# Kernel optimization log

Hardware: AMD Instinct MI355X
Metric: run time of the kernel (lower is better)

Reference implementation:

```python
import jax, jax.numpy as jnp
import numpy as np

BETA = 0.3        # SmoothL1Loss beta
LAMBDA_PHY = 0.15 # physics loss weight


def smooth_l1(d, beta):
    ad = jnp.abs(d)
    return jnp.where(ad < beta, 0.5 * d * d / beta, ad - 0.5 * beta)


def setup_inputs() -> dict:
    key = jax.random.key(0)
    k1, k2, k3, k4 = jax.random.split(key, 4)
    B, Z = 16384, 2048
    preds = jax.random.normal(k1, (B, Z, 1), dtype=jnp.float32)
    targets = jax.random.normal(k2, (B, Z), dtype=jnp.float32)
    current_temps = jax.random.normal(k3, (B, Z), dtype=jnp.float32)
    adjacency = jax.random.randint(k4, (Z, Z), 0, 2).astype(jnp.int32)
    return {"preds": preds, "targets": targets,
            "current_temps": current_temps, "adjacency": adjacency}


def reference(preds, targets, current_temps, adjacency):
    p = preds[:, :, 0]                               # [B, Z]
    num_zones = p.shape[1]
    pred_loss = smooth_l1(p - targets, BETA).mean()
    pred_change = p - current_temps                  # [B, Z]

    # Vectorized neighbor mean: replaces the per-zone Python loop with one
    # dense masked-adjacency contraction.
    mask = (adjacency > 0).astype(p.dtype)           # [Z, Z]
    deg = mask.sum(axis=1)                           # [Z]
    has_nb = deg > 0
    safe_deg = jnp.where(has_nb, deg, 1.0)
    avg_neighbor = jnp.einsum('zn,bn->bz', mask, current_temps) / safe_deg  # [B, Z]

    temp_diff = current_temps - avg_neighbor         # [B, Z]
    violation = jax.nn.softplus(temp_diff * pred_change)
    per_zone = violation.mean(axis=0)                # mean over batch, [Z]
    physics_loss = jnp.where(has_nb, per_zone, 0.0).sum() / num_zones

    total_loss = pred_loss + LAMBDA_PHY * physics_loss
    return (total_loss, physics_loss)
```

## Files before the change

### kernel.cpp

```cpp
#include <hip/hip_runtime.h>
#include <hip/hip_bf16.h>
#include <cmath>

#define BETA 0.3f
#define LAMBDA_PHY 0.15f

#define BM 128
#define BN 128
#define BK 64
#define NT 512

typedef __bf16 bf16x8 __attribute__((ext_vector_type(8)));
typedef float f32x4 __attribute__((ext_vector_type(4)));

#define AS1 __attribute__((address_space(1)))
#define AS3 __attribute__((address_space(3)))

#define FENCE() asm volatile("" ::: "memory")
#define BARRIER() do { FENCE(); __builtin_amdgcn_s_barrier(); FENCE(); } while (0)
#define WAITV4() asm volatile("s_waitcnt vmcnt(4)" ::: "memory")
#define WAITV0() asm volatile("s_waitcnt vmcnt(0)" ::: "memory")

__device__ __forceinline__ unsigned short f2bf_rn(float f) {
    unsigned int u = __builtin_bit_cast(unsigned int, f);
    return (unsigned short)((u + 0x7FFFu + ((u >> 16) & 1u)) >> 16);
}

__device__ __forceinline__ float bf2f(unsigned short u) {
    return __builtin_bit_cast(float, (unsigned int)u << 16);
}

__device__ __forceinline__ float softplus_f(float x) {
    return fmaxf(x, 0.0f) + __logf(1.0f + __expf(-fabsf(x)));
}

__device__ __forceinline__ float smooth_l1_f(float d) {
    float ad = fabsf(d);
    return (ad < BETA) ? (0.5f / BETA) * d * d : (ad - 0.5f * BETA);
}

__global__ void k_prep(const int* __restrict__ adj, unsigned short* __restrict__ maskbf,
                       float* __restrict__ invdeg, float* __restrict__ hasnb, int Z) {
    int z = blockIdx.x;
    int t = threadIdx.x;
    const int* row = adj + (size_t)z * Z;
    unsigned short* mrow = maskbf + (size_t)z * Z;
    int cnt = 0;
    for (int n = t; n < Z; n += blockDim.x) {
        int a = (row[n] > 0);
        mrow[n] = a ? (unsigned short)0x3F80 : (unsigned short)0;
        cnt += a;
    }
    for (int o = 32; o; o >>= 1) cnt += __shfl_down(cnt, o);
    __shared__ int rs[4];
    int lane = t & 63, wave = t >> 6;
    if (lane == 0) rs[wave] = cnt;
    __syncthreads();
    if (t == 0) {
        int deg = rs[0] + rs[1] + rs[2] + rs[3];
        invdeg[z] = (deg > 0) ? 1.0f / (float)deg : 1.0f;
        hasnb[z]  = (deg > 0) ? 1.0f : 0.0f;
    }
}

__global__ void k_conv(const float* __restrict__ src, uint4* __restrict__ dst, long n8) {
    long i = (long)blockIdx.x * blockDim.x + threadIdx.x;
    long stride = (long)gridDim.x * blockDim.x;
    for (; i < n8; i += stride) {
        const float4* s = (const float4*)(src + i * 8);
        float4 a = s[0], b = s[1];
        uint4 o;
        o.x = (unsigned)f2bf_rn(a.x) | ((unsigned)f2bf_rn(a.y) << 16);
        o.y = (unsigned)f2bf_rn(a.z) | ((unsigned)f2bf_rn(a.w) << 16);
        o.z = (unsigned)f2bf_rn(b.x) | ((unsigned)f2bf_rn(b.y) << 16);
        o.w = (unsigned)f2bf_rn(b.z) | ((unsigned)f2bf_rn(b.w) << 16);
        dst[i] = o;
    }
}

__global__ __launch_bounds__(NT, 4) void k_gemm(
    const unsigned short* __restrict__ Abf,
    const unsigned short* __restrict__ Bbf,
    const float* __restrict__ preds,
    const float* __restrict__ targets,
    const float* __restrict__ invdeg,
    const float* __restrict__ hasnb,
    float* __restrict__ partials,
    int M, int N, int K)
{
    __shared__ unsigned short As[2][BM * 64];
    __shared__ unsigned short Bs[2][BN * 64];

    const int nwg = gridDim.x;
    const int ob = blockIdx.x;
    const int bid = (nwg % 8 == 0) ? ((ob % 8) * (nwg / 8) + ob / 8) : ob;
    const int ntiles = N / BN;
    const int mt = bid / ntiles;
    const int nt = bid % ntiles;
    const int row0 = mt * BM;
    const int col0 = nt * BN;
    const int t = threadIdx.x;
    const int lane = t & 63;
    const int wave = t >> 6;
    const int wm = wave >> 2;
    const int wn = wave & 3;
    const int fr = lane & 15;
    const int fq = lane >> 4;
    const int fr7 = fr & 7;

    const int tr = t >> 3;
    const int tc = t & 7;
    const int cs = tc ^ (tr & 7);

    f32x4 acc[4][2];
#pragma unroll
    for (int m = 0; m < 4; ++m)
#pragma unroll
        for (int n = 0; n < 2; ++n)
            acc[m][n] = (f32x4){0.f, 0.f, 0.f, 0.f};

    const unsigned short* aSrc = Abf + (size_t)(row0 + tr) * K + cs * 8;
    const unsigned short* bSrc = Bbf + (size_t)(col0 + tr) * K + cs * 8;
    unsigned short* aDst = &As[0][t * 8];
    unsigned short* bDst = &Bs[0][t * 8];

#define STAGE4(nbuf) do {                                                                    \
    unsigned short* ad_ = aDst + (nbuf) * (BM * 64);                                         \
    unsigned short* bd_ = bDst + (nbuf) * (BN * 64);                                         \
    _Pragma("unroll")                                                                        \
    for (int r_ = 0; r_ < 2; ++r_)                                                           \
        __builtin_amdgcn_global_load_lds((const AS1 void*)(aSrc + (size_t)(r_ * 64) * K),    \
                                         (AS3 void*)(ad_ + r_ * 4096), 16, 0, 0);            \
    _Pragma("unroll")                                                                        \
    for (int r_ = 0; r_ < 2; ++r_)                                                           \
        __builtin_amdgcn_global_load_lds((const AS1 void*)(bSrc + (size_t)(r_ * 64) * K),    \
                                         (AS3 void*)(bd_ + r_ * 4096), 16, 0, 0);            \
} while (0)

#define MFMA_TILE(buf) do {                                                                  \
    _Pragma("unroll")                                                                        \
    for (int kk_ = 0; kk_ < 2; ++kk_) {                                                      \
        bf16x8 af_[4], bv_[2];                                                               \
        _Pragma("unroll")                                                                    \
        for (int mi_ = 0; mi_ < 4; ++mi_)                                                    \
            af_[mi_] = *(const bf16x8*)&As[buf][(wm * 64 + mi_ * 16 + fr) * 64 +             \
                                               (((kk_ * 4 + fq) ^ fr7) * 8)];                \
        _Pragma("unroll")                                                                    \
        for (int ni_ = 0; ni_ < 2; ++ni_)                                                    \
            bv_[ni_] = *(const bf16x8*)&Bs[buf][(wn * 32 + ni_ * 16 + fr) * 64 +             \
                                               (((kk_ * 4 + fq) ^ fr7) * 8)];                \
        _Pragma("unroll")                                                                    \
        for (int mi_ = 0; mi_ < 4; ++mi_)                                                    \
        _Pragma("unroll")                                                                    \
        for (int ni_ = 0; ni_ < 2; ++ni_)                                                    \
            acc[mi_][ni_] = __builtin_amdgcn_mfma_f32_16x16x32_bf16(                         \
                af_[mi_], bv_[ni_], acc[mi_][ni_], 0, 0, 0);                                 \
    }                                                                                        \
} while (0)

    const int nk = K / BK;
    STAGE4(0);
    aSrc += BK; bSrc += BK;

    int cur = 0;
    for (int ti = 0; ti < nk; ++ti) {
        if (ti + 1 < nk) {
            STAGE4(cur ^ 1);
            aSrc += BK; bSrc += BK;
            WAITV4();
        } else {
            WAITV0();
        }
        BARRIER();
        MFMA_TILE(cur);
        BARRIER();
        cur ^= 1;
    }

#undef STAGE4
#undef MFMA_TILE

    float vsum = 0.f, ssum = 0.f;
#pragma unroll
    for (int n = 0; n < 2; ++n) {
        const int z = col0 + wn * 32 + n * 16 + fr;
        const float idg = invdeg[z];
        const float hnb = hasnb[z];
#pragma unroll
        for (int m = 0; m < 4; ++m) {
            const int rb = row0 + wm * 64 + m * 16 + fq * 4;
#pragma unroll
            for (int j = 0; j < 4; ++j) {
                const size_t idx = (size_t)(rb + j) * N + z;
                float avg = acc[m][n][j] * idg;
                float c = bf2f(Abf[idx]);
                float p = preds[idx];
                float tg = targets[idx];
                float x = (c - avg) * (p - c);
                vsum += softplus_f(x) * hnb;
                ssum += smooth_l1_f(p - tg);
            }
        }
    }
    for (int o = 32; o; o >>= 1) { vsum += __shfl_down(vsum, o); ssum += __shfl_down(ssum, o); }
    __shared__ float rv[8], rsm[8];
    if (lane == 0) { rv[wave] = vsum; rsm[wave] = ssum; }
    __syncthreads();
    if (t == 0) {
        float v = 0.f, s = 0.f;
#pragma unroll
        for (int w = 0; w < 8; ++w) { v += rv[w]; s += rsm[w]; }
        partials[2 * (size_t)ob]     = v;
        partials[2 * (size_t)ob + 1] = s;
    }
}

__global__ void k_finalize(const float* __restrict__ partials, int nblk,
                           float* __restrict__ out, float invBZ) {
    __shared__ float sv[256], ss[256];
    int t = threadIdx.x;
    float v = 0.f, s = 0.f;
    for (int i = t; i < nblk; i += 256) { v += partials[2 * (size_t)i]; s += partials[2 * (size_t)i + 1]; }
    sv[t] = v; ss[t] = s;
    __syncthreads();
    for (int o = 128; o; o >>= 1) {
        if (t < o) { sv[t] += sv[t + o]; ss[t] += ss[t + o]; }
        __syncthreads();
    }
    if (t == 0) {
        float phys = sv[0] * invBZ;
        float pred = ss[0] * invBZ;
        out[0] = pred + LAMBDA_PHY * phys;
        out[1] = phys;
    }
}

__global__ void k_zero2(float* p) { if (threadIdx.x < 2) p[threadIdx.x] = 0.f; }

__global__ void k_fallback(const float* __restrict__ preds, const float* __restrict__ targets,
                           const float* __restrict__ ctemps, const int* __restrict__ adj,
                           float* __restrict__ acc2, int B, int Z) {
    extern __shared__ float crow[];
    int nzb = (Z + 255) / 256;
    int b = blockIdx.x / nzb;
    int zb = blockIdx.x % nzb;
    int t = threadIdx.x;
    const float* cr = ctemps + (size_t)b * Z;
    for (int n = t; n < Z; n += 256) crow[n] = cr[n];
    __syncthreads();
    int z = zb * 256 + t;
    float vsum = 0.f, ssum = 0.f;
    if (z < Z) {
        const int* arow = adj + (size_t)z * Z;
        float sum = 0.f; int deg = 0;
        for (int n = 0; n < Z; ++n) {
            if (arow[n] > 0) { sum += crow[n]; ++deg; }
        }
        float avg = (deg > 0) ? sum / (float)deg : 0.f;
        float c = crow[z];
        size_t idx = (size_t)b * Z + z;
        float p = preds[idx];
        float x = (c - avg) * (p - c);
        vsum = (deg > 0) ? softplus_f(x) : 0.f;
        ssum = smooth_l1_f(p - targets[idx]);
    }
    for (int o = 32; o; o >>= 1) { vsum += __shfl_down(vsum, o); ssum += __shfl_down(ssum, o); }
    __shared__ float rv[4], rs2[4];
    int lane = t & 63, wave = t >> 6;
    if (lane == 0) { rv[wave] = vsum; rs2[wave] = ssum; }
    __syncthreads();
    if (t == 0) {
        atomicAdd(&acc2[0], rv[0] + rv[1] + rv[2] + rv[3]);
        atomicAdd(&acc2[1], rs2[0] + rs2[1] + rs2[2] + rs2[3]);
    }
}

extern "C" void kernel_launch(void* const* d_in, const int* in_sizes, int n_in,
                              void* d_out, int out_size, void* d_ws, size_t ws_size,
                              hipStream_t stream) {
    const float* preds   = (const float*)d_in[0];
    const float* targets = (const float*)d_in[1];
    const float* ctemps  = (const float*)d_in[2];
    const int*   adj     = (const int*)d_in[3];
    float* out = (float*)d_out;

    long zz = in_sizes[3];
    int Z = (int)llround(sqrt((double)zz));
    int B = in_sizes[1] / Z;

    size_t off = 0;
    size_t maskOff = off; off += (size_t)Z * Z * 2;
    size_t cbfOff  = off; off += (size_t)B * Z * 2;
    size_t idgOff  = off; off += (size_t)Z * 4;
    size_t hnbOff  = off; off += (size_t)Z * 4;
    int nblk = (Z > 0 && B > 0 && (B % BM) == 0 && (Z % BN) == 0) ? (B / BM) * (Z / BN) : 0;
    size_t partOff = off; off += (size_t)(nblk > 0 ? nblk : 1) * 2 * 4;

    bool main_ok = (B % BM == 0) && (Z % BN == 0) && (Z % BK == 0) && (ws_size >= off);

    float invBZ = (float)(1.0 / ((double)B * (double)Z));

    if (main_ok) {
        char* ws = (char*)d_ws;
        unsigned short* maskbf = (unsigned short*)(ws + maskOff);
        unsigned short* cbf    = (unsigned short*)(ws + cbfOff);
        float* idg      = (float*)(ws + idgOff);
        float* hnb      = (float*)(ws + hnbOff);
        float* partials = (float*)(ws + partOff);

        k_prep<<<Z, 256, 0, stream>>>(adj, maskbf, idg, hnb, Z);
        long n8 = (long)B * Z / 8;
        k_conv<<<2048, 256, 0, stream>>>(ctemps, (uint4*)cbf, n8);
        k_gemm<<<nblk, NT, 0, stream>>>(cbf, maskbf, preds, targets, idg, hnb, partials, B, Z, Z);
        k_finalize<<<1, 256, 0, stream>>>(partials, nblk, out, invBZ);
    } else {
        float* acc2 = (float*)d_ws;
        k_zero2<<<1, 64, 0, stream>>>(acc2);
        int nzb = (Z + 255) / 256;
        k_fallback<<<B * nzb, 256, (size_t)Z * 4, stream>>>(preds, targets, ctemps, adj, acc2, B, Z);
        k_finalize<<<1, 256, 0, stream>>>(acc2, 1, out, invBZ);
    }
}
```

Measured before the change: 233.5 us.

## Switch GEMM operands to FP8 e4m3 and fuse prep with conversion kernel

Converts current_temps and the adjacency mask to FP8 e4m3 instead of bf16 and uses fp8 MFMA with a K tile of 128 bytes. It also merges the mask-prep and conversion kernels into one launch, unrolls the double-buffer loop by two, and raises wave priority around MFMA issue. The aim is to halve the operand bytes and conversion write traffic and to use the higher fp8 MFMA throughput. In exchange, current_temps loses a lot of precision (3 mantissa bits), which affects both the neighbor mean and the violation term and may push the loss outside tolerance.

```diff
diff --git a/kernel.cpp b/kernel.cpp
--- a/kernel.cpp
+++ b/kernel.cpp
@@ -7,10 +7,9 @@
 
 #define BM 128
 #define BN 128
-#define BK 64
+#define BKE 128
 #define NT 512
 
-typedef __bf16 bf16x8 __attribute__((ext_vector_type(8)));
 typedef float f32x4 __attribute__((ext_vector_type(4)));
 
 #define AS1 __attribute__((address_space(1)))
@@ -21,15 +20,6 @@
 #define WAITV4() asm volatile("s_waitcnt vmcnt(4)" ::: "memory")
 #define WAITV0() asm volatile("s_waitcnt vmcnt(0)" ::: "memory")
 
-__device__ __forceinline__ unsigned short f2bf_rn(float f) {
-    unsigned int u = __builtin_bit_cast(unsigned int, f);
-    return (unsigned short)((u + 0x7FFFu + ((u >> 16) & 1u)) >> 16);
-}
-
-__device__ __forceinline__ float bf2f(unsigned short u) {
-    return __builtin_bit_cast(float, (unsigned int)u << 16);
-}
-
 __device__ __forceinline__ float softplus_f(float x) {
     return fmaxf(x, 0.0f) + __logf(1.0f + __expf(-fabsf(x)));
 }
@@ -39,48 +29,77 @@
     return (ad < BETA) ? (0.5f / BETA) * d * d : (ad - 0.5f * BETA);
 }
 
-__global__ void k_prep(const int* __restrict__ adj, unsigned short* __restrict__ maskbf,
-                       float* __restrict__ invdeg, float* __restrict__ hasnb, int Z) {
-    int z = blockIdx.x;
+__device__ __forceinline__ unsigned f_e4m3(float f) {
+    unsigned u = __builtin_bit_cast(unsigned, f);
+    unsigned s = (u >> 24) & 0x80u;
+    unsigned ab = u & 0x7fffffffu;
+    float a = __builtin_bit_cast(float, ab);
+    if (a >= 448.f) return s | 0x7Eu;
+    if (a < 0.015625f) {
+        int q = (int)rintf(a * 512.f);
+        return s | (unsigned)q;
+    }
+    unsigned r = ab + 0x7FFFFu + ((ab >> 20) & 1u);
+    unsigned ee = (r >> 23) - 120u;
+    unsigned m = (r >> 20) & 7u;
+    return s | (ee << 3) | m;
+}
+
+__device__ __forceinline__ float e4m3_f(unsigned v) {
+    unsigned em = v & 0x7fu;
+    float nrm = __builtin_bit_cast(float, (em << 20) + 0x3C000000u);
+    float sub = (float)em * 0.001953125f;
+    float r = (em >= 8u) ? nrm : sub;
+    unsigned sb = (v & 0x80u) << 24;
+    return __builtin_bit_cast(float, __builtin_bit_cast(unsigned, r) | sb);
+}
+
+__global__ void k_prepconv(const int* __restrict__ adj, unsigned char* __restrict__ maskf8,
+                           float* __restrict__ invdeg, float* __restrict__ hasnb, int Z,
+                           const float* __restrict__ src, uint4* __restrict__ dst,
+                           long n16, int ncb) {
     int t = threadIdx.x;
-    const int* row = adj + (size_t)z * Z;
-    unsigned short* mrow = maskbf + (size_t)z * Z;
-    int cnt = 0;
-    for (int n = t; n < Z; n += blockDim.x) {
-        int a = (row[n] > 0);
-        mrow[n] = a ? (unsigned short)0x3F80 : (unsigned short)0;
-        cnt += a;
-    }
-    for (int o = 32; o; o >>= 1) cnt += __shfl_down(cnt, o);
-    __shared__ int rs[4];
-    int lane = t & 63, wave = t >> 6;
-    if (lane == 0) rs[wave] = cnt;
-    __syncthreads();
-    if (t == 0) {
-        int deg = rs[0] + rs[1] + rs[2] + rs[3];
-        invdeg[z] = (deg > 0) ? 1.0f / (float)deg : 1.0f;
-        hasnb[z]  = (deg > 0) ? 1.0f : 0.0f;
-    }
-}
-
-__global__ void k_conv(const float* __restrict__ src, uint4* __restrict__ dst, long n8) {
-    long i = (long)blockIdx.x * blockDim.x + threadIdx.x;
-    long stride = (long)gridDim.x * blockDim.x;
-    for (; i < n8; i += stride) {
-        const float4* s = (const float4*)(src + i * 8);
-        float4 a = s[0], b = s[1];
-        uint4 o;
-        o.x = (unsigned)f2bf_rn(a.x) | ((unsigned)f2bf_rn(a.y) << 16);
-        o.y = (unsigned)f2bf_rn(a.z) | ((unsigned)f2bf_rn(a.w) << 16);
-        o.z = (unsigned)f2bf_rn(b.x) | ((unsigned)f2bf_rn(b.y) << 16);
-        o.w = (unsigned)f2bf_rn(b.z) | ((unsigned)f2bf_rn(b.w) << 16);
-        dst[i] = o;
+    if ((int)blockIdx.x < Z) {
+        int z = blockIdx.x;
+        const int* row = adj + (size_t)z * Z;
+        unsigned char* mrow = maskf8 + (size_t)z * Z;
+        int cnt = 0;
+        for (int n = t; n < Z; n += blockDim.x) {
+            int a = (row[n] > 0);
+            mrow[n] = a ? (unsigned char)0x38 : (unsigned char)0;
+            cnt += a;
+        }
+        for (int o = 32; o; o >>= 1) cnt += __shfl_down(cnt, o);
+        __shared__ int rs[4];
+        int lane = t & 63, wave = t >> 6;
+        if (lane == 0) rs[wave] = cnt;
+        __syncthreads();
+        if (t == 0) {
+            int deg = rs[0] + rs[1] + rs[2] + rs[3];
+            invdeg[z] = (deg > 0) ? 1.0f / (float)deg : 1.0f;
+            hasnb[z]  = (deg > 0) ? 1.0f : 0.0f;
+        }
+    } else {
+        long i = (long)(blockIdx.x - Z) * blockDim.x + t;
+        long stride = (long)ncb * blockDim.x;
+        for (; i < n16; i += stride) {
+            const float4* s = (const float4*)(src + i * 16);
+            uint4 o;
+            unsigned w[4];
+#pragma unroll
+            for (int q = 0; q < 4; ++q) {
+                float4 v = s[q];
+                w[q] = f_e4m3(v.x) | (f_e4m3(v.y) << 8) | (f_e4m3(v.z) << 16) | (f_e4m3(v.w) << 24);
+            }
+            o.x = w[0]; o.y = w[1]; o.z = w[2]; o.w = w[3];
+            dst[i] = o;
+        }
     }
 }
 
 __global__ __launch_bounds__(NT, 4) void k_gemm(
-    const unsigned short* __restrict__ Abf,
-    const unsigned short* __restrict__ Bbf,
+    const unsigned char* __restrict__ Af8,
+    const unsigned char* __restrict__ Bf8,
     const float* __restrict__ preds,
     const float* __restrict__ targets,
     const float* __restrict__ invdeg,
@@ -88,8 +107,8 @@
     float* __restrict__ partials,
     int M, int N, int K)
 {
-    __shared__ unsigned short As[2][BM * 64];
-    __shared__ unsigned short Bs[2][BN * 64];
+    __shared__ __align__(16) unsigned char AsF[2 * BM * BKE];
+    __shared__ __align__(16) unsigned char BsF[2 * BN * BKE];
 
     const int nwg = gridDim.x;
     const int ob = blockIdx.x;
@@ -112,6 +131,14 @@
     const int tc = t & 7;
     const int cs = tc ^ (tr & 7);
 
+    int ofsA[4], ofsB[4];
+#pragma unroll
+    for (int kk = 0; kk < 4; ++kk) {
+        const int sp = (((2 * kk + (fq >> 1)) ^ fr7) << 4) + (fq & 1) * 8;
+        ofsA[kk] = (wm * 64 + fr) * BKE + sp;
+        ofsB[kk] = (wn * 32 + fr) * BKE + sp;
+    }
+
     f32x4 acc[4][2];
 #pragma unroll
     for (int m = 0; m < 4; ++m)
@@ -119,65 +146,66 @@
         for (int n = 0; n < 2; ++n)
             acc[m][n] = (f32x4){0.f, 0.f, 0.f, 0.f};
 
-    const unsigned short* aSrc = Abf + (size_t)(row0 + tr) * K + cs * 8;
-    const unsigned short* bSrc = Bbf + (size_t)(col0 + tr) * K + cs * 8;
-    unsigned short* aDst = &As[0][t * 8];
-    unsigned short* bDst = &Bs[0][t * 8];
-
-#define STAGE4(nbuf) do {                                                                    \
-    unsigned short* ad_ = aDst + (nbuf) * (BM * 64);                                         \
-    unsigned short* bd_ = bDst + (nbuf) * (BN * 64);                                         \
+    const unsigned char* aSrc = Af8 + (size_t)(row0 + tr) * K + cs * 16;
+    const unsigned char* bSrc = Bf8 + (size_t)(col0 + tr) * K + cs * 16;
+    unsigned char* aDstC = &AsF[t * 16];
+    unsigned char* bDstC = &BsF[t * 16];
+
+#define STAGE(BUF) do {                                                                      \
+    __builtin_amdgcn_global_load_lds((const AS1 void*)(aSrc),                                \
+                                     (AS3 void*)(aDstC + (BUF) * 16384), 16, 0, 0);          \
+    __builtin_amdgcn_global_load_lds((const AS1 void*)(aSrc + (size_t)64 * K),               \
+                                     (AS3 void*)(aDstC + (BUF) * 16384 + 8192), 16, 0, 0);   \
+    __builtin_amdgcn_global_load_lds((const AS1 void*)(bSrc),                                \
+                                     (AS3 void*)(bDstC + (BUF) * 16384), 16, 0, 0);          \
+    __builtin_amdgcn_global_load_lds((const AS1 void*)(bSrc + (size_t)64 * K),               \
+                                     (AS3 void*)(bDstC + (BUF) * 16384 + 8192), 16, 0, 0);   \
+    aSrc += BKE; bSrc += BKE;                                                                \
+} while (0)
+
+#define MFMA_TILE(BUF) do {                                                                  \
     _Pragma("unroll")                                                                        \
-    for (int r_ = 0; r_ < 2; ++r_)                                                           \
-        __builtin_amdgcn_global_load_lds((const AS1 void*)(aSrc + (size_t)(r_ * 64) * K),    \
-                                         (AS3 void*)(ad_ + r_ * 4096), 16, 0, 0);            \
-    _Pragma("unroll")                                                                        \
-    for (int r_ = 0; r_ < 2; ++r_)                                                           \
-        __builtin_amdgcn_global_load_lds((const AS1 void*)(bSrc + (size_t)(r_ * 64) * K),    \
-                                         (AS3 void*)(bd_ + r_ * 4096), 16, 0, 0);            \
-} while (0)
-
-#define MFMA_TILE(buf) do {                                                                  \
-    _Pragma("unroll")                                                                        \
-    for (int kk_ = 0; kk_ < 2; ++kk_) {                                                      \
-        bf16x8 af_[4], bv_[2];                                                               \
+    for (int kk_ = 0; kk_ < 4; ++kk_) {                                                      \
+        long af_[4], bv_[2];                                                                 \
         _Pragma("unroll")                                                                    \
         for (int mi_ = 0; mi_ < 4; ++mi_)                                                    \
-            af_[mi_] = *(const bf16x8*)&As[buf][(wm * 64 + mi_ * 16 + fr) * 64 +             \
-                                               (((kk_ * 4 + fq) ^ fr7) * 8)];                \
+            af_[mi_] = *(const long*)(AsF + (BUF) * 16384 + ofsA[kk_] + mi_ * 2048);         \
         _Pragma("unroll")                                                                    \
         for (int ni_ = 0; ni_ < 2; ++ni_)                                                    \
-            bv_[ni_] = *(const bf16x8*)&Bs[buf][(wn * 32 + ni_ * 16 + fr) * 64 +             \
-                                               (((kk_ * 4 + fq) ^ fr7) * 8)];                \
+            bv_[ni_] = *(const long*)(BsF + (BUF) * 16384 + ofsB[kk_] + ni_ * 2048);         \
+        __builtin_amdgcn_s_setprio(1);                                                       \
         _Pragma("unroll")                                                                    \
         for (int mi_ = 0; mi_ < 4; ++mi_)                                                    \
         _Pragma("unroll")                                                                    \
         for (int ni_ = 0; ni_ < 2; ++ni_)                                                    \
-            acc[mi_][ni_] = __builtin_amdgcn_mfma_f32_16x16x32_bf16(                         \
+            acc[mi_][ni_] = __builtin_amdgcn_mfma_f32_16x16x32_fp8_fp8(                      \
                 af_[mi_], bv_[ni_], acc[mi_][ni_], 0, 0, 0);                                 \
+        __builtin_amdgcn_s_setprio(0);                                                       \
     }                                                                                        \
 } while (0)
 
-    const int nk = K / BK;
-    STAGE4(0);
-    aSrc += BK; bSrc += BK;
-
-    int cur = 0;
-    for (int ti = 0; ti < nk; ++ti) {
-        if (ti + 1 < nk) {
-            STAGE4(cur ^ 1);
-            aSrc += BK; bSrc += BK;
+    const int nk = K / BKE;
+    const int nk2 = nk >> 1;
+    STAGE(0);
+
+    for (int i = 0; i < nk2; ++i) {
+        STAGE(1);
+        WAITV4();
+        BARRIER();
+        MFMA_TILE(0);
+        BARRIER();
+        if (i + 1 < nk2) {
+            STAGE(0);
             WAITV4();
         } else {
             WAITV0();
         }
         BARRIER();
-        MFMA_TILE(cur);
+        MFMA_TILE(1);
         BARRIER();
-        cur ^= 1;
-    }
-
-#undef STAGE4
+    }
+
+#undef STAGE
 #undef MFMA_TILE
 
     float vsum = 0.f, ssum = 0.f;
@@ -193,7 +221,7 @@
             for (int j = 0; j < 4; ++j) {
                 const size_t idx = (size_t)(rb + j) * N + z;
                 float avg = acc[m][n][j] * idg;
-                float c = bf2f(Abf[idx]);
+                float c = e4m3_f(Af8[idx]);
                 float p = preds[idx];
                 float tg = targets[idx];
                 float x = (c - avg) * (p - c);
@@ -289,29 +317,31 @@
     int B = in_sizes[1] / Z;
 
     size_t off = 0;
-    size_t maskOff = off; off += (size_t)Z * Z * 2;
-    size_t cbfOff  = off; off += (size_t)B * Z * 2;
+    size_t maskOff = off; off += (size_t)Z * Z;
+    size_t cf8Off  = off; off += (size_t)B * Z;
     size_t idgOff  = off; off += (size_t)Z * 4;
     size_t hnbOff  = off; off += (size_t)Z * 4;
     int nblk = (Z > 0 && B > 0 && (B % BM) == 0 && (Z % BN) == 0) ? (B / BM) * (Z / BN) : 0;
     size_t partOff = off; off += (size_t)(nblk > 0 ? nblk : 1) * 2 * 4;
 
-    bool main_ok = (B % BM == 0) && (Z % BN == 0) && (Z % BK == 0) && (ws_size >= off);
+    bool main_ok = (B % BM == 0) && (Z % BN == 0) && (Z % BKE == 0) &&
+                   (((Z / BKE) % 2) == 0) && ((B * Z) % 16 == 0) && (ws_size >= off);
 
     float invBZ = (float)(1.0 / ((double)B * (double)Z));
 
     if (main_ok) {
         char* ws = (char*)d_ws;
-        unsigned short* maskbf = (unsigned short*)(ws + maskOff);
-        unsigned short* cbf    = (unsigned short*)(ws + cbfOff);
+        unsigned char* maskf8 = (unsigned char*)(ws + maskOff);
+        unsigned char* cf8    = (unsigned char*)(ws + cf8Off);
         float* idg      = (float*)(ws + idgOff);
         float* hnb      = (float*)(ws + hnbOff);
         float* partials = (float*)(ws + partOff);
 
-        k_prep<<<Z, 256, 0, stream>>>(adj, maskbf, idg, hnb, Z);
-        long n8 = (long)B * Z / 8;
-        k_conv<<<2048, 256, 0, stream>>>(ctemps, (uint4*)cbf, n8);
-        k_gemm<<<nblk, NT, 0, stream>>>(cbf, maskbf, preds, targets, idg, hnb, partials, B, Z, Z);
+        long n16 = (long)B * Z / 16;
+        int ncb = 2048;
+        k_prepconv<<<Z + ncb, 256, 0, stream>>>(adj, maskf8, idg, hnb, Z,
+                                                ctemps, (uint4*)cf8, n16, ncb);
+        k_gemm<<<nblk, NT, 0, stream>>>(cf8, maskf8, preds, targets, idg, hnb, partials, B, Z, Z);
         k_finalize<<<1, 256, 0, stream>>>(partials, nblk, out, invBZ);
     } else {
         float* acc2 = (float*)d_ws;
```

Measured after the change: 202.1 us. 13.4% less time.
